# Performance work log

Hardware: AMD Instinct MI355X
Metric: run time of the kernel (lower is better)

Reference implementation:

```python
import jax, jax.numpy as jnp
import numpy as np

B, N, W, H = 2, 2048, 1024, 16
HD = W // H  # head dim = 64
STD = 0.02


def setup_inputs() -> dict:
    key = jax.random.key(0)
    ks = jax.random.split(key, 8)
    x = jax.random.normal(ks[0], (B, N, W), dtype=jnp.float32)
    # weights stored [in, out] (transposed vs torch nn.Linear)
    qkv_w = jax.random.normal(ks[1], (W, 3 * W), dtype=jnp.float32) * STD
    qkv_b = jnp.zeros((3 * W,), jnp.float32)
    proj_w = jax.random.normal(ks[2], (W, W), dtype=jnp.float32) * STD
    proj_b = jnp.zeros((W,), jnp.float32)
    fc_w = jax.random.normal(ks[3], (W, 4 * W), dtype=jnp.float32) * STD
    fc_b = jnp.zeros((4 * W,), jnp.float32)
    fc2_w = jax.random.normal(ks[4], (4 * W, W), dtype=jnp.float32) * STD
    fc2_b = jnp.zeros((W,), jnp.float32)
    ln1_g = jnp.ones((W,), jnp.float32)
    ln1_b = jnp.zeros((W,), jnp.float32)
    ln2_g = jnp.ones((W,), jnp.float32)
    ln2_b = jnp.zeros((W,), jnp.float32)
    return dict(x=x, ln1_g=ln1_g, ln1_b=ln1_b, qkv_w=qkv_w, qkv_b=qkv_b,
                proj_w=proj_w, proj_b=proj_b, ln2_g=ln2_g, ln2_b=ln2_b,
                fc_w=fc_w, fc_b=fc_b, fc2_w=fc2_w, fc2_b=fc2_b)


def _layernorm(x, g, b, eps=1e-5):
    mu = jnp.mean(x, axis=-1, keepdims=True)
    var = jnp.var(x, axis=-1, keepdims=True)
    return (x - mu) * jax.lax.rsqrt(var + eps) * g + b


def _attention(x, qkv_w, qkv_b, proj_w, proj_b):
    bs, n, w = x.shape
    qkv = x @ qkv_w + qkv_b                      # [b, n, 3W]
    qkv = qkv.reshape(bs, n, H, 3 * HD)
    q, k, v = jnp.split(qkv, 3, axis=-1)         # each [b, n, h, hd]
    scale = 1.0 / np.sqrt(np.sqrt(HD)).astype(np.float32)
    # hand-rolled attention: full [b, h, t, s] score matrix, fp32 softmax
    weight = jnp.einsum('bthc,bshc->bhts', q * scale, k * scale)
    weight = jax.nn.softmax(weight.astype(jnp.float32), axis=-1).astype(weight.dtype)
    out = jnp.einsum('bhts,bshc->bthc', weight, v).reshape(bs, n, w)
    return out @ proj_w + proj_b


def reference(x, ln1_g, ln1_b, qkv_w, qkv_b, proj_w, proj_b,
              ln2_g, ln2_b, fc_w, fc_b, fc2_w, fc2_b):
    x = x + _attention(_layernorm(x, ln1_g, ln1_b), qkv_w, qkv_b, proj_w, proj_b)
    h = _layernorm(x, ln2_g, ln2_b)
    h = jax.nn.gelu(h @ fc_w + fc_b, approximate=False) @ fc2_w + fc2_b
    return x + h
```

## Files before the change

kernel.cpp:

```cpp
#include <hip/hip_runtime.h>
#include <hip/hip_bf16.h>
#include <type_traits>
#include <cstdint>

using bf16 = __hip_bfloat16;
typedef __attribute__((ext_vector_type(8))) short bf16x8;
typedef __attribute__((ext_vector_type(4))) float f32x4;

__device__ __forceinline__ float bf2f(unsigned short u) {
    union { unsigned int i; float f; } c; c.i = ((unsigned int)u) << 16; return c.f;
}

#define GLLDS16(gp, lp)                                                          \
    __builtin_amdgcn_global_load_lds(                                            \
        (const __attribute__((address_space(1))) void*)(gp),                     \
        (__attribute__((address_space(3))) void*)(lp), 16, 0, 0)

__global__ __launch_bounds__(256) void transpose_f2b(const float* __restrict__ w,
                                                     bf16* __restrict__ wt,
                                                     int K, int N) {
    __shared__ bf16 t[32][33];
    const int tid = threadIdx.x;
    const int n0 = blockIdx.x * 32, k0 = blockIdx.y * 32;
#pragma unroll
    for (int i = 0; i < 4; ++i) {
        int idx = tid + i * 256;
        int r = idx >> 5, c = idx & 31;
        t[r][c] = __float2bfloat16(w[(size_t)(k0 + r) * N + n0 + c]);
    }
    __syncthreads();
#pragma unroll
    for (int i = 0; i < 4; ++i) {
        int idx = tid + i * 256;
        int r = idx >> 5, c = idx & 31;
        wt[(size_t)(n0 + r) * K + k0 + c] = t[c][r];
    }
}

__global__ __launch_bounds__(256) void vtrans_kernel(const bf16* __restrict__ qkv,
                                                     bf16* __restrict__ vtg) {
    __shared__ bf16 t[32][33];
    const int tid = threadIdx.x;
    const int s0 = blockIdx.x * 32, c0 = blockIdx.y * 32;
    const int bh = blockIdx.z, b = bh >> 4, h = bh & 15;
#pragma unroll
    for (int i = 0; i < 4; ++i) {
        int idx = tid + i * 256;
        int r = idx >> 5, c = idx & 31;
        t[r][c] = qkv[(size_t)(b * 2048 + s0 + r) * 3072 + h * 192 + 128 + c0 + c];
    }
    __syncthreads();
#pragma unroll
    for (int i = 0; i < 4; ++i) {
        int idx = tid + i * 256;
        int r = idx >> 5, c = idx & 31;
        vtg[((size_t)bh * 64 + c0 + r) * 2048 + s0 + c] = t[c][r];
    }
}

template <typename InT>
__global__ __launch_bounds__(256) void ln_kernel(const InT* __restrict__ x,
                                                 const float* __restrict__ g,
                                                 const float* __restrict__ bta,
                                                 bf16* __restrict__ y) {
    const int row = blockIdx.x, tid = threadIdx.x;
    const size_t base = (size_t)row * 1024 + tid * 4;
    float v[4];
    if constexpr (std::is_same_v<InT, float>) {
        float4 f = *(const float4*)(x + base);
        v[0] = f.x; v[1] = f.y; v[2] = f.z; v[3] = f.w;
    } else {
        ushort4 u = *(const ushort4*)((const unsigned short*)x + base);
        v[0] = bf2f(u.x); v[1] = bf2f(u.y); v[2] = bf2f(u.z); v[3] = bf2f(u.w);
    }
    float s = v[0] + v[1] + v[2] + v[3];
    float sq = v[0]*v[0] + v[1]*v[1] + v[2]*v[2] + v[3]*v[3];
#pragma unroll
    for (int off = 32; off > 0; off >>= 1) {
        s  += __shfl_down(s, off);
        sq += __shfl_down(sq, off);
    }
    __shared__ float red[8];
    const int wave = tid >> 6, lane = tid & 63;
    if (lane == 0) { red[wave] = s; red[4 + wave] = sq; }
    __syncthreads();
    s  = red[0] + red[1] + red[2] + red[3];
    sq = red[4] + red[5] + red[6] + red[7];
    const float mu   = s * (1.0f / 1024.0f);
    const float var  = sq * (1.0f / 1024.0f) - mu * mu;
    const float rstd = rsqrtf(var + 1e-5f);
#pragma unroll
    for (int e = 0; e < 4; ++e) {
        int col = tid * 4 + e;
        float yy = (v[e] - mu) * rstd * g[col] + bta[col];
        y[base + e] = __float2bfloat16(yy);
    }
}

template <int EPI, int BM>
__global__ __launch_bounds__(256) void gemm_kernel(const bf16* __restrict__ A,
                                                   const bf16* __restrict__ Bt,
                                                   const float* __restrict__ bias,
                                                   const void* __restrict__ resid,
                                                   void* __restrict__ Cout,
                                                   int M, int N, int K) {
    constexpr int IF = 4;
    constexpr int JF = (BM == 128) ? 4 : 2;
    constexpr bool GL = (BM == 128);
    constexpr int ST = GL ? 64 : 72;
    __shared__ __align__(16) bf16 As[BM * ST];
    __shared__ __align__(16) bf16 Bs[128 * ST];
    const int tid  = threadIdx.x;
    const int wave = tid >> 6, lane = tid & 63;
    const int quad = lane >> 4, l16 = lane & 15;
    const int wm = GL ? (wave >> 1) * 64 : 0;
    const int wn = GL ? (wave & 1) * 64 : wave * 32;
    const int bm = blockIdx.y * BM, bn = blockIdx.x * 128;

    int kz0 = 0, kz1 = K;
    if constexpr (EPI == 4) {
        kz0 = blockIdx.z * (K >> 1);
        kz1 = kz0 + (K >> 1);
    }

    const int r8 = lane >> 3, sc = lane & 7;
    const bf16* ag = A  + (size_t)(bm + wave * 8 + r8) * K + ((sc ^ r8) << 3);
    const bf16* bg = Bt + (size_t)(bn + wave * 8 + r8) * K + ((sc ^ r8) << 3);

    f32x4 acc[IF][JF];
#pragma unroll
    for (int i = 0; i < IF; ++i)
#pragma unroll
        for (int j = 0; j < JF; ++j) acc[i][j] = (f32x4){0.f, 0.f, 0.f, 0.f};

    for (int kt = kz0; kt < kz1; kt += 64) {
        __syncthreads();
        if constexpr (GL) {
#pragma unroll
            for (int i = 0; i < 4; ++i) {
                GLLDS16(ag + (size_t)(i * 32) * K + kt, &As[(wave * 8 + i * 32) * 64]);
                GLLDS16(bg + (size_t)(i * 32) * K + kt, &Bs[(wave * 8 + i * 32) * 64]);
            }
        } else {
#pragma unroll
            for (int i = 0; i < BM * 8 / 256; ++i) {
                int c0 = tid + i * 256;
                int r = c0 >> 3, kc = (c0 & 7) << 3;
                *(uint4*)(&As[r * ST + kc]) = *(const uint4*)(A + (size_t)(bm + r) * K + kt + kc);
            }
#pragma unroll
            for (int i = 0; i < 4; ++i) {
                int c0 = tid + i * 256;
                int r = c0 >> 3, kc = (c0 & 7) << 3;
                *(uint4*)(&Bs[r * ST + kc]) = *(const uint4*)(Bt + (size_t)(bn + r) * K + kt + kc);
            }
        }
        __syncthreads();
#pragma unroll
        for (int ks = 0; ks < 2; ++ks) {
            bf16x8 af[IF], bfr[JF];
            if constexpr (GL) {
                const int swr = l16 & 7;
#pragma unroll
                for (int i = 0; i < IF; ++i)
                    af[i] = *(const bf16x8*)(&As[(wm + i * 16 + l16) * 64 +
                                                 (((ks * 4 + quad) ^ swr) << 3)]);
#pragma unroll
                for (int j = 0; j < JF; ++j)
                    bfr[j] = *(const bf16x8*)(&Bs[(wn + j * 16 + l16) * 64 +
                                                  (((ks * 4 + quad) ^ swr) << 3)]);
            } else {
#pragma unroll
                for (int i = 0; i < IF; ++i)
                    af[i] = *(const bf16x8*)(&As[(wm + i * 16 + l16) * ST + ks * 32 + quad * 8]);
#pragma unroll
                for (int j = 0; j < JF; ++j)
                    bfr[j] = *(const bf16x8*)(&Bs[(wn + j * 16 + l16) * ST + ks * 32 + quad * 8]);
            }
#pragma unroll
            for (int i = 0; i < IF; ++i)
#pragma unroll
                for (int j = 0; j < JF; ++j)
                    acc[i][j] = __builtin_amdgcn_mfma_f32_16x16x32_bf16(af[i], bfr[j], acc[i][j], 0, 0, 0);
        }
    }
    float* skdst = nullptr;
    if constexpr (EPI == 4)
        skdst = blockIdx.z ? (float*)const_cast<void*>(resid) : (float*)Cout;
#pragma unroll
    for (int i = 0; i < IF; ++i) {
#pragma unroll
        for (int j = 0; j < JF; ++j) {
#pragma unroll
            for (int r = 0; r < 4; ++r) {
                const int row = bm + wm + i * 16 + quad * 4 + r;
                const int col = bn + wn + j * 16 + l16;
                float v = acc[i][j][r];
                if constexpr (EPI != 4) v += bias[col];
                if constexpr (EPI == 1)
                    v = 0.5f * v * (1.0f + erff(v * 0.70710678118654752f));
                if constexpr (EPI == 2) {
                    v += ((const float*)resid)[(size_t)row * N + col];
                    ((bf16*)Cout)[(size_t)row * N + col] = __float2bfloat16(v);
                } else if constexpr (EPI == 3) {
                    v += bf2f(((const unsigned short*)resid)[(size_t)row * N + col]);
                    ((float*)Cout)[(size_t)row * N + col] = v;
                } else if constexpr (EPI == 4) {
                    skdst[(size_t)row * N + col] = v;
                } else {
                    ((bf16*)Cout)[(size_t)row * N + col] = __float2bfloat16(v);
                }
            }
        }
    }
}

__global__ __launch_bounds__(256) void merge_fc2(const float* __restrict__ p0,
                                                 const float* __restrict__ p1,
                                                 const float* __restrict__ bias,
                                                 const bf16* __restrict__ resid,
                                                 float* __restrict__ outp) {
    const int idx = blockIdx.x * 256 + threadIdx.x;
    const int row = idx >> 8, col = (idx & 255) * 4;
    const size_t off = (size_t)row * 1024 + col;
    float4 a = *(const float4*)(p0 + off);
    float4 b = *(const float4*)(p1 + off);
    float4 bs = *(const float4*)(bias + col);
    ushort4 r = *(const ushort4*)((const unsigned short*)resid + off);
    float4 o;
    o.x = a.x + b.x + bs.x + bf2f(r.x);
    o.y = a.y + b.y + bs.y + bf2f(r.y);
    o.z = a.z + b.z + bs.z + bf2f(r.z);
    o.w = a.w + b.w + bs.w + bf2f(r.w);
    *(float4*)(outp + off) = o;
}

__global__ __launch_bounds__(256) void attn_kernel(const bf16* __restrict__ qkv,
                                                   const bf16* __restrict__ vtg,
                                                   bf16* __restrict__ Opart,
                                                   float* __restrict__ Lp) {
    __shared__ __align__(16) bf16 Ks[64 * 64];
    __shared__ __align__(16) bf16 Vs[64 * 64];
    __shared__ __align__(16) bf16 Ps[4][2][16][72];
    const int tid  = threadIdx.x;
    const int wave = tid >> 6, lane = tid & 63;
    const int quad = lane >> 4, l16 = lane & 15;
    const int qt = blockIdx.x, h = blockIdx.y;
    const int b = blockIdx.z >> 1, seg = blockIdx.z & 1;
    const size_t tok0 = (size_t)b * 2048;
    const int qbase = qt * 128 + wave * 32;

    bf16x8 qf[2][2];
#pragma unroll
    for (int set = 0; set < 2; ++set) {
        const bf16* qp = qkv + (tok0 + qbase + set * 16 + l16) * 3072 + h * 192 + quad * 8;
        qf[set][0] = *(const bf16x8*)(qp);
        qf[set][1] = *(const bf16x8*)(qp + 32);
    }

    const int swc = ((tid & 7) ^ ((tid >> 3) & 7)) * 8;
    const bf16* kg = qkv + (tok0 + (tid >> 3)) * 3072 + h * 192 + 64 + swc;
    const bf16* vg = vtg + ((size_t)(b * 16 + h) * 64 + (tid >> 3)) * 2048 + swc;

    const short oneb = 0x3f80;
    const bf16x8 ones = {oneb, oneb, oneb, oneb, oneb, oneb, oneb, oneb};

    f32x4 o[2][4], l_acc[2];
#pragma unroll
    for (int set = 0; set < 2; ++set) {
        l_acc[set] = (f32x4){0.f, 0.f, 0.f, 0.f};
#pragma unroll
        for (int j = 0; j < 4; ++j) o[set][j] = (f32x4){0.f, 0.f, 0.f, 0.f};
    }

    const int kt0 = seg * 1024;
    for (int kt = kt0; kt < kt0 + 1024; kt += 64) {
        __syncthreads();
        GLLDS16(kg + (size_t)kt * 3072,        &Ks[(wave * 64) * 8]);
        GLLDS16(kg + (size_t)(kt + 32) * 3072, &Ks[(wave * 64 + 256) * 8]);
        GLLDS16(vg + kt,                       &Vs[(wave * 64) * 8]);
        GLLDS16(vg + kt + 32 * 2048,           &Vs[(wave * 64 + 256) * 8]);
        __syncthreads();

#pragma unroll
        for (int j = 0; j < 4; ++j) {
            const int rk = j * 16 + l16;
            const int sw = l16 & 7;
            bf16x8 kb0 = *(const bf16x8*)(&Ks[rk * 64 + ((quad ^ sw) * 8)]);
            bf16x8 kb1 = *(const bf16x8*)(&Ks[rk * 64 + (((quad + 4) ^ sw) * 8)]);
#pragma unroll
            for (int set = 0; set < 2; ++set) {
                f32x4 s4 = (f32x4){0.f, 0.f, 0.f, 0.f};
                s4 = __builtin_amdgcn_mfma_f32_16x16x32_bf16(qf[set][0], kb0, s4, 0, 0, 0);
                s4 = __builtin_amdgcn_mfma_f32_16x16x32_bf16(qf[set][1], kb1, s4, 0, 0, 0);
#pragma unroll
                for (int r = 0; r < 4; ++r)
                    Ps[wave][set][quad * 4 + r][j * 16 + l16] =
                        __float2bfloat16(__expf(s4[r] * 0.125f));
            }
        }
#pragma unroll
        for (int kk = 0; kk < 2; ++kk) {
            bf16x8 pf0 = *(const bf16x8*)(&Ps[wave][0][l16][kk * 32 + quad * 8]);
            bf16x8 pf1 = *(const bf16x8*)(&Ps[wave][1][l16][kk * 32 + quad * 8]);
            l_acc[0] = __builtin_amdgcn_mfma_f32_16x16x32_bf16(pf0, ones, l_acc[0], 0, 0, 0);
            l_acc[1] = __builtin_amdgcn_mfma_f32_16x16x32_bf16(pf1, ones, l_acc[1], 0, 0, 0);
#pragma unroll
            for (int j = 0; j < 4; ++j) {
                const int rv = j * 16 + l16;
                bf16x8 vf = *(const bf16x8*)(&Vs[rv * 64 + (((kk * 4 + quad) ^ (l16 & 7)) * 8)]);
                o[0][j] = __builtin_amdgcn_mfma_f32_16x16x32_bf16(pf0, vf, o[0][j], 0, 0, 0);
                o[1][j] = __builtin_amdgcn_mfma_f32_16x16x32_bf16(pf1, vf, o[1][j], 0, 0, 0);
            }
        }
    }
    const size_t segoff = (size_t)seg * 4096;
#pragma unroll
    for (int set = 0; set < 2; ++set)
#pragma unroll
        for (int j = 0; j < 4; ++j)
#pragma unroll
            for (int r = 0; r < 4; ++r) {
                int row = qbase + set * 16 + quad * 4 + r;
                Opart[(segoff + tok0 + row) * 1024 + h * 64 + j * 16 + l16] =
                    __float2bfloat16(o[set][j][r]);
            }
    if (l16 == 0) {
#pragma unroll
        for (int set = 0; set < 2; ++set)
#pragma unroll
            for (int r = 0; r < 4; ++r) {
                int row = qbase + set * 16 + quad * 4 + r;
                Lp[(segoff + tok0 + row) * 16 + h] = l_acc[set][r];
            }
    }
}

__global__ __launch_bounds__(256) void merge_kernel(const bf16* __restrict__ Opart,
                                                    const float* __restrict__ Lp,
                                                    bf16* __restrict__ outp) {
    const int idx = blockIdx.x * 256 + threadIdx.x;
    const int c4 = idx & 15, h = (idx >> 4) & 15, gt = idx >> 8;
    const size_t li0 = (size_t)gt * 16 + h, li1 = li0 + 4096 * 16;
    float inv = 1.0f / (Lp[li0] + Lp[li1]);
    const size_t off = (size_t)gt * 1024 + h * 64 + c4 * 4;
    ushort4 a = *(const ushort4*)((const unsigned short*)Opart + off);
    ushort4 bb = *(const ushort4*)((const unsigned short*)Opart + off + (size_t)4096 * 1024);
    float va[4] = {bf2f(a.x), bf2f(a.y), bf2f(a.z), bf2f(a.w)};
    float vb[4] = {bf2f(bb.x), bf2f(bb.y), bf2f(bb.z), bf2f(bb.w)};
    unsigned short res[4];
#pragma unroll
    for (int e = 0; e < 4; ++e) {
        bf16 o = __float2bfloat16((va[e] + vb[e]) * inv);
        res[e] = *(unsigned short*)&o;
    }
    *(ushort4*)((unsigned short*)outp + off) = make_ushort4(res[0], res[1], res[2], res[3]);
}

extern "C" void kernel_launch(void* const* d_in, const int* in_sizes, int n_in,
                              void* d_out, int out_size, void* d_ws, size_t ws_size,
                              hipStream_t stream) {
    const float* x      = (const float*)d_in[0];
    const float* ln1_g  = (const float*)d_in[1];
    const float* ln1_b  = (const float*)d_in[2];
    const float* qkv_w  = (const float*)d_in[3];
    const float* qkv_b  = (const float*)d_in[4];
    const float* proj_w = (const float*)d_in[5];
    const float* proj_b = (const float*)d_in[6];
    const float* ln2_g  = (const float*)d_in[7];
    const float* ln2_b  = (const float*)d_in[8];
    const float* fc_w   = (const float*)d_in[9];
    const float* fc_b   = (const float*)d_in[10];
    const float* fc2_w  = (const float*)d_in[11];
    const float* fc2_b  = (const float*)d_in[12];
    float* outp = (float*)d_out;

    char* ws = (char*)d_ws;
    const size_t MB = 1024 * 1024;
    bf16*  wfcT   = (bf16*)(ws + 0 * MB);
    float* part1  = (float*)(ws + 0 * MB);
    bf16*  lnbuf  = (bf16*)(ws + 8 * MB);
    bf16*  wprojT = (bf16*)(ws + 8 * MB);
    float* Lp     = (float*)(ws + 10 * MB);
    bf16*  wqkvT  = (bf16*)(ws + 16 * MB);
    bf16*  vtg    = (bf16*)(ws + 16 * MB);
    bf16*  attnout= (bf16*)(ws + 16 * MB);
    bf16*  fcact  = (bf16*)(ws + 16 * MB);
    bf16*  qkvb   = (bf16*)(ws + 24 * MB);
    bf16*  Opart  = (bf16*)(ws + 48 * MB);
    bf16*  wfc2T  = (bf16*)(ws + 48 * MB);
    bf16*  x1     = (bf16*)(ws + 56 * MB);

    transpose_f2b<<<dim3(96, 32),  256, 0, stream>>>(qkv_w, wqkvT, 1024, 3072);
    transpose_f2b<<<dim3(128, 32), 256, 0, stream>>>(fc_w,  wfcT,  1024, 4096);
    ln_kernel<float><<<4096, 256, 0, stream>>>(x, ln1_g, ln1_b, lnbuf);
    gemm_kernel<0, 128><<<dim3(24, 32), 256, 0, stream>>>(lnbuf, wqkvT, qkv_b, nullptr, qkvb, 4096, 3072, 1024);
    vtrans_kernel<<<dim3(64, 2, 32), 256, 0, stream>>>(qkvb, vtg);
    transpose_f2b<<<dim3(32, 32), 256, 0, stream>>>(proj_w, wprojT, 1024, 1024);
    attn_kernel<<<dim3(16, 16, 4), 256, 0, stream>>>(qkvb, vtg, Opart, Lp);
    merge_kernel<<<4096, 256, 0, stream>>>(Opart, Lp, attnout);
    transpose_f2b<<<dim3(32, 128), 256, 0, stream>>>(fc2_w, wfc2T, 4096, 1024);
    gemm_kernel<2, 64><<<dim3(8, 64), 256, 0, stream>>>(attnout, wprojT, proj_b, x, x1, 4096, 1024, 1024);
    ln_kernel<bf16><<<4096, 256, 0, stream>>>(x1, ln2_g, ln2_b, lnbuf);
    gemm_kernel<1, 128><<<dim3(32, 32), 256, 0, stream>>>(lnbuf, wfcT, fc_b, nullptr, fcact, 4096, 4096, 1024);
    gemm_kernel<4, 64><<<dim3(8, 64, 2), 256, 0, stream>>>(fcact, wfc2T, nullptr, part1, outp, 4096, 1024, 4096);
    merge_fc2<<<4096, 256, 0, stream>>>(outp, part1, fc2_b, x1, outp);
}
```

Before: 376.2 us.

## Double-buffer LDS tiles in GEMM and attention, use polynomial GELU

Adds double-buffered shared-memory tiles to the global_load_lds GEMM path and to the attention K/V staging, so the next tile's loads are issued before computing on the current one and one barrier per iteration is removed. It also replaces erff in the GELU epilogue with an Abramowitz-Stegun polynomial approximation using a fast reciprocal, and raises wave priority around the PV MFMA block. The cost is doubled LDS use, which may reduce occupancy, and a GELU approximation with max error around 1e-7 relative to erf.

```diff
diff --git a/kernel.cpp b/kernel.cpp
--- a/kernel.cpp
+++ b/kernel.cpp
@@ -9,6 +9,17 @@
 
 __device__ __forceinline__ float bf2f(unsigned short u) {
     union { unsigned int i; float f; } c; c.i = ((unsigned int)u) << 16; return c.f;
+}
+
+__device__ __forceinline__ float gelu_f(float v) {
+    float x  = v * 0.70710678118654752f;
+    float ax = fabsf(x);
+    float t  = __builtin_amdgcn_rcpf(1.0f + 0.3275911f * ax);
+    float poly = ((((1.061405429f * t - 1.453152027f) * t + 1.421413741f) * t
+                   - 0.284496736f) * t + 0.254829592f) * t;
+    float erfv = 1.0f - poly * __expf(-ax * ax);
+    erfv = copysignf(erfv, x);
+    return 0.5f * v * (1.0f + erfv);
 }
 
 #define GLLDS16(gp, lp)                                                          \
@@ -108,8 +119,9 @@
     constexpr int JF = (BM == 128) ? 4 : 2;
     constexpr bool GL = (BM == 128);
     constexpr int ST = GL ? 64 : 72;
-    __shared__ __align__(16) bf16 As[BM * ST];
-    __shared__ __align__(16) bf16 Bs[128 * ST];
+    constexpr int NB = GL ? 2 : 1;
+    __shared__ __align__(16) bf16 As[NB][BM * ST];
+    __shared__ __align__(16) bf16 Bs[NB][128 * ST];
     const int tid  = threadIdx.x;
     const int wave = tid >> 6, lane = tid & 63;
     const int quad = lane >> 4, l16 = lane & 15;
@@ -133,55 +145,74 @@
 #pragma unroll
         for (int j = 0; j < JF; ++j) acc[i][j] = (f32x4){0.f, 0.f, 0.f, 0.f};
 
-    for (int kt = kz0; kt < kz1; kt += 64) {
+    if constexpr (GL) {
+        auto stage = [&](int buf, int kt) {
+#pragma unroll
+            for (int i = 0; i < 4; ++i) {
+                GLLDS16(ag + (size_t)(i * 32) * K + kt, &As[buf][(wave * 8 + i * 32) * 64]);
+                GLLDS16(bg + (size_t)(i * 32) * K + kt, &Bs[buf][(wave * 8 + i * 32) * 64]);
+            }
+        };
+        auto compute = [&](int buf) {
+#pragma unroll
+            for (int ks = 0; ks < 2; ++ks) {
+                bf16x8 af[IF], bfr[JF];
+                const int swr = l16 & 7;
+#pragma unroll
+                for (int i = 0; i < IF; ++i)
+                    af[i] = *(const bf16x8*)(&As[buf][(wm + i * 16 + l16) * 64 +
+                                                      (((ks * 4 + quad) ^ swr) << 3)]);
+#pragma unroll
+                for (int j = 0; j < JF; ++j)
+                    bfr[j] = *(const bf16x8*)(&Bs[buf][(wn + j * 16 + l16) * 64 +
+                                                       (((ks * 4 + quad) ^ swr) << 3)]);
+#pragma unroll
+                for (int i = 0; i < IF; ++i)
+#pragma unroll
+                    for (int j = 0; j < JF; ++j)
+                        acc[i][j] = __builtin_amdgcn_mfma_f32_16x16x32_bf16(af[i], bfr[j], acc[i][j], 0, 0, 0);
+            }
+        };
+        stage(0, kz0);
         __syncthreads();
-        if constexpr (GL) {
-#pragma unroll
-            for (int i = 0; i < 4; ++i) {
-                GLLDS16(ag + (size_t)(i * 32) * K + kt, &As[(wave * 8 + i * 32) * 64]);
-                GLLDS16(bg + (size_t)(i * 32) * K + kt, &Bs[(wave * 8 + i * 32) * 64]);
-            }
-        } else {
+        int cur = 0;
+        for (int kt = kz0; kt < kz1; kt += 64) {
+            if (kt + 64 < kz1) stage(cur ^ 1, kt + 64);
+            compute(cur);
+            __syncthreads();
+            cur ^= 1;
+        }
+    } else {
+        for (int kt = kz0; kt < kz1; kt += 64) {
+            __syncthreads();
 #pragma unroll
             for (int i = 0; i < BM * 8 / 256; ++i) {
                 int c0 = tid + i * 256;
                 int r = c0 >> 3, kc = (c0 & 7) << 3;
-                *(uint4*)(&As[r * ST + kc]) = *(const uint4*)(A + (size_t)(bm + r) * K + kt + kc);
+                *(uint4*)(&As[0][r * ST + kc]) = *(const uint4*)(A + (size_t)(bm + r) * K + kt + kc);
             }
 #pragma unroll
             for (int i = 0; i < 4; ++i) {
                 int c0 = tid + i * 256;
                 int r = c0 >> 3, kc = (c0 & 7) << 3;
-                *(uint4*)(&Bs[r * ST + kc]) = *(const uint4*)(Bt + (size_t)(bn + r) * K + kt + kc);
-            }
-        }
-        __syncthreads();
-#pragma unroll
-        for (int ks = 0; ks < 2; ++ks) {
-            bf16x8 af[IF], bfr[JF];
-            if constexpr (GL) {
-                const int swr = l16 & 7;
+                *(uint4*)(&Bs[0][r * ST + kc]) = *(const uint4*)(Bt + (size_t)(bn + r) * K + kt + kc);
+            }
+            __syncthreads();
+#pragma unroll
+            for (int ks = 0; ks < 2; ++ks) {
+                bf16x8 af[IF], bfr[JF];
 #pragma unroll
                 for (int i = 0; i < IF; ++i)
-                    af[i] = *(const bf16x8*)(&As[(wm + i * 16 + l16) * 64 +
-                                                 (((ks * 4 + quad) ^ swr) << 3)]);
+                    af[i] = *(const bf16x8*)(&As[0][(wm + i * 16 + l16) * ST + ks * 32 + quad * 8]);
 #pragma unroll
                 for (int j = 0; j < JF; ++j)
-                    bfr[j] = *(const bf16x8*)(&Bs[(wn + j * 16 + l16) * 64 +
-                                                  (((ks * 4 + quad) ^ swr) << 3)]);
-            } else {
+                    bfr[j] = *(const bf16x8*)(&Bs[0][(wn + j * 16 + l16) * ST + ks * 32 + quad * 8]);
 #pragma unroll
                 for (int i = 0; i < IF; ++i)
-                    af[i] = *(const bf16x8*)(&As[(wm + i * 16 + l16) * ST + ks * 32 + quad * 8]);
-#pragma unroll
-                for (int j = 0; j < JF; ++j)
-                    bfr[j] = *(const bf16x8*)(&Bs[(wn + j * 16 + l16) * ST + ks * 32 + quad * 8]);
-            }
-#pragma unroll
-            for (int i = 0; i < IF; ++i)
-#pragma unroll
-                for (int j = 0; j < JF; ++j)
-                    acc[i][j] = __builtin_amdgcn_mfma_f32_16x16x32_bf16(af[i], bfr[j], acc[i][j], 0, 0, 0);
+#pragma unroll
+                    for (int j = 0; j < JF; ++j)
+                        acc[i][j] = __builtin_amdgcn_mfma_f32_16x16x32_bf16(af[i], bfr[j], acc[i][j], 0, 0, 0);
+            }
         }
     }
     float* skdst = nullptr;
@@ -198,7 +229,7 @@
                 float v = acc[i][j][r];
                 if constexpr (EPI != 4) v += bias[col];
                 if constexpr (EPI == 1)
-                    v = 0.5f * v * (1.0f + erff(v * 0.70710678118654752f));
+                    v = gelu_f(v);
                 if constexpr (EPI == 2) {
                     v += ((const float*)resid)[(size_t)row * N + col];
                     ((bf16*)Cout)[(size_t)row * N + col] = __float2bfloat16(v);
@@ -239,8 +270,8 @@
                                                    const bf16* __restrict__ vtg,
                                                    bf16* __restrict__ Opart,
                                                    float* __restrict__ Lp) {
-    __shared__ __align__(16) bf16 Ks[64 * 64];
-    __shared__ __align__(16) bf16 Vs[64 * 64];
+    __shared__ __align__(16) bf16 Ks[2][64 * 64];
+    __shared__ __align__(16) bf16 Vs[2][64 * 64];
     __shared__ __align__(16) bf16 Ps[4][2][16][72];
     const int tid  = threadIdx.x;
     const int wave = tid >> 6, lane = tid & 63;
@@ -273,21 +304,26 @@
         for (int j = 0; j < 4; ++j) o[set][j] = (f32x4){0.f, 0.f, 0.f, 0.f};
     }
 
+    auto stageKV = [&](int buf, int kt) {
+        GLLDS16(kg + (size_t)kt * 3072,        &Ks[buf][(wave * 64) * 8]);
+        GLLDS16(kg + (size_t)(kt + 32) * 3072, &Ks[buf][(wave * 64 + 256) * 8]);
+        GLLDS16(vg + kt,                       &Vs[buf][(wave * 64) * 8]);
+        GLLDS16(vg + kt + 32 * 2048,           &Vs[buf][(wave * 64 + 256) * 8]);
+    };
+
     const int kt0 = seg * 1024;
+    stageKV(0, kt0);
+    __syncthreads();
+    int cur = 0;
     for (int kt = kt0; kt < kt0 + 1024; kt += 64) {
-        __syncthreads();
-        GLLDS16(kg + (size_t)kt * 3072,        &Ks[(wave * 64) * 8]);
-        GLLDS16(kg + (size_t)(kt + 32) * 3072, &Ks[(wave * 64 + 256) * 8]);
-        GLLDS16(vg + kt,                       &Vs[(wave * 64) * 8]);
-        GLLDS16(vg + kt + 32 * 2048,           &Vs[(wave * 64 + 256) * 8]);
-        __syncthreads();
+        if (kt + 64 < kt0 + 1024) stageKV(cur ^ 1, kt + 64);
 
 #pragma unroll
         for (int j = 0; j < 4; ++j) {
             const int rk = j * 16 + l16;
             const int sw = l16 & 7;
-            bf16x8 kb0 = *(const bf16x8*)(&Ks[rk * 64 + ((quad ^ sw) * 8)]);
-            bf16x8 kb1 = *(const bf16x8*)(&Ks[rk * 64 + (((quad + 4) ^ sw) * 8)]);
+            bf16x8 kb0 = *(const bf16x8*)(&Ks[cur][rk * 64 + ((quad ^ sw) * 8)]);
+            bf16x8 kb1 = *(const bf16x8*)(&Ks[cur][rk * 64 + (((quad + 4) ^ sw) * 8)]);
 #pragma unroll
             for (int set = 0; set < 2; ++set) {
                 f32x4 s4 = (f32x4){0.f, 0.f, 0.f, 0.f};
@@ -299,6 +335,7 @@
                         __float2bfloat16(__expf(s4[r] * 0.125f));
             }
         }
+        __builtin_amdgcn_s_setprio(1);
 #pragma unroll
         for (int kk = 0; kk < 2; ++kk) {
             bf16x8 pf0 = *(const bf16x8*)(&Ps[wave][0][l16][kk * 32 + quad * 8]);
@@ -308,11 +345,14 @@
 #pragma unroll
             for (int j = 0; j < 4; ++j) {
                 const int rv = j * 16 + l16;
-                bf16x8 vf = *(const bf16x8*)(&Vs[rv * 64 + (((kk * 4 + quad) ^ (l16 & 7)) * 8)]);
+                bf16x8 vf = *(const bf16x8*)(&Vs[cur][rv * 64 + (((kk * 4 + quad) ^ (l16 & 7)) * 8)]);
                 o[0][j] = __builtin_amdgcn_mfma_f32_16x16x32_bf16(pf0, vf, o[0][j], 0, 0, 0);
                 o[1][j] = __builtin_amdgcn_mfma_f32_16x16x32_bf16(pf1, vf, o[1][j], 0, 0, 0);
             }
         }
+        __builtin_amdgcn_s_setprio(0);
+        __syncthreads();
+        cur ^= 1;
     }
     const size_t segoff = (size_t)seg * 4096;
 #pragma unroll
```

New measurement: 386.8 us. 1.03x slower.
